# Performance work log

Measured on AMD Instinct MI355X. Metric: run time of the kernel, lower is better.

The kernel has to match this reference:

```python
import jax, jax.numpy as jnp
import numpy as np

B, T, DM = 2, 2048, 1024
H, HKV, DH = 16, 4, 64          # n_heads, n_kv_heads, head_dim
LAT, DFF = 64, 4096             # MLA latent dim, SwiGLU hidden (4*d_model)
SCALE = DH ** -0.5
ROPE_BASE = 10000.0


def _rope(x):
    # x: [B, T, h, DH]; split-half rotary
    half = DH // 2
    pos = jnp.arange(T, dtype=jnp.float32)
    inv_freq = 1.0 / (ROPE_BASE ** (jnp.arange(half, dtype=jnp.float32) / half))
    ang = pos[:, None] * inv_freq                      # [T, half]
    cos = jnp.cos(ang)[None, :, None, :]
    sin = jnp.sin(ang)[None, :, None, :]
    x1, x2 = x[..., :half], x[..., half:]
    return jnp.concatenate([x1 * cos - x2 * sin, x2 * cos + x1 * sin], axis=-1)


def setup_inputs() -> dict:
    key = jax.random.key(0)
    ks = jax.random.split(key, 9)
    init = lambda k, shape, fan: jax.random.normal(k, shape, jnp.float32) * (fan ** -0.5)
    return {
        "x": jax.random.normal(ks[0], (B, T, DM), jnp.float32),
        "Wq": init(ks[1], (DM, DM), DM),
        "Wkv_down": init(ks[2], (DM, LAT), DM),
        "Wk_up": init(ks[3], (LAT, HKV * DH), LAT),
        "Wv_up": init(ks[4], (LAT, HKV * DH), LAT),
        "Wgate": init(ks[5], (DH, DH), DH),
        "bgate": jnp.zeros((DH,), jnp.float32),
        "Wo1": init(ks[6], (DM, DFF), DM),
        "Wo2": init(ks[7], (DFF, DM), DFF),
    }


def reference(x, Wq, Wkv_down, Wk_up, Wv_up, Wgate, bgate, Wo1, Wo2):
    # GQA projections; MLA: shared low-rank latent -> K/V up-projections
    q = (x @ Wq).reshape(B, T, H, DH)
    lat = x @ Wkv_down                                  # [B, T, LAT]
    k = (lat @ Wk_up).reshape(B, T, HKV, DH)
    v = (lat @ Wv_up).reshape(B, T, HKV, DH)

    q = _rope(q)
    k = _rope(k)

    # repeat KV heads (GQA): kv head g serves q heads [g*rep, (g+1)*rep)
    rep = H // HKV
    k = jnp.repeat(k, rep, axis=2)                      # [B, T, H, DH]
    v = jnp.repeat(v, rep, axis=2)

    scores = jnp.einsum("bthd,bshd->bhts", q, k) * SCALE
    causal = jnp.tril(jnp.ones((T, T), dtype=bool))
    scores = jnp.where(causal[None, None], scores, -jnp.inf)
    attn = jax.nn.softmax(scores, axis=-1)
    out = jnp.einsum("bhts,bshd->bthd", attn, v)        # [B, T, H, DH]

    # Gated attention (G1, per_head): sigmoid gate after attention
    gate = jax.nn.sigmoid(out @ Wgate + bgate)
    out = (out * gate).reshape(B, T, DM)

    # SwiGLU-style out_proj: Linear -> SiLU -> Linear
    h = jax.nn.silu(out @ Wo1)
    return h @ Wo2
```

## Files before the change

kernel.cpp:

```cpp
#include <hip/hip_runtime.h>
#include <math.h>

#define NB 2
#define NT 2048
#define NDM 1024
#define NH 16
#define NHKV 4
#define NDH 64
#define NLAT 64
#define NDFF 4096

typedef __attribute__((ext_vector_type(4))) float fx4;
typedef __attribute__((ext_vector_type(8))) short bf8;
typedef __attribute__((ext_vector_type(4))) unsigned short us4;
typedef __attribute__((ext_vector_type(8))) unsigned short us8;

__device__ __forceinline__ unsigned short f2bf(float f) {
  union { float f; unsigned int u; } v; v.f = f;
  unsigned int u = v.u;
  u += 0x7fffu + ((u >> 16) & 1u);
  return (unsigned short)(u >> 16);
}

__global__ void conv_bf_k(const float* __restrict__ in,
                          unsigned short* __restrict__ out, int n8) {
  int idx = blockIdx.x * 256 + threadIdx.x;
  if (idx >= n8) return;
  fx4 a = *(const fx4*)(in + (size_t)idx * 8);
  fx4 b = *(const fx4*)(in + (size_t)idx * 8 + 4);
  us8 o = { f2bf(a[0]), f2bf(a[1]), f2bf(a[2]), f2bf(a[3]),
            f2bf(b[0]), f2bf(b[1]), f2bf(b[2]), f2bf(b[3]) };
  *(us8*)(out + (size_t)idx * 8) = o;
}

__global__ __launch_bounds__(256) void convT_bf_k(const float* __restrict__ W,
                                                  unsigned short* __restrict__ Wt,
                                                  int K, int N) {
  __shared__ float tile[64 * 65];
  const int t = threadIdx.x;
  const int k0 = blockIdx.x * 64, n0 = blockIdx.y * 64;
#pragma unroll
  for (int i = 0; i < 4; ++i) {
    int id = t + 256 * i;
    int row = id >> 4, c = (id & 15) * 4;
    fx4 v = *(const fx4*)(W + (size_t)(k0 + row) * N + n0 + c);
    tile[row * 65 + c + 0] = v[0];
    tile[row * 65 + c + 1] = v[1];
    tile[row * 65 + c + 2] = v[2];
    tile[row * 65 + c + 3] = v[3];
  }
  __syncthreads();
  const int nr = t >> 2, kc = (t & 3) * 16;
  us8 o0, o1;
#pragma unroll
  for (int e = 0; e < 8; ++e) o0[e] = f2bf(tile[(kc + e) * 65 + nr]);
#pragma unroll
  for (int e = 0; e < 8; ++e) o1[e] = f2bf(tile[(kc + 8 + e) * 65 + nr]);
  *(us8*)(Wt + (size_t)(n0 + nr) * K + k0 + kc) = o0;
  *(us8*)(Wt + (size_t)(n0 + nr) * K + k0 + kc + 8) = o1;
}

template<int EPI>
__global__ __launch_bounds__(256) void gemm_bf_k(const unsigned short* __restrict__ A,
                                                 const unsigned short* __restrict__ Bt,
                                                 void* __restrict__ Cp,
                                                 int M, int N, int K) {
  __shared__ unsigned short As[128 * 72];
  __shared__ unsigned short Bs[128 * 72];
  const int t = threadIdx.x;
  const int m0 = blockIdx.x * 128, n0 = blockIdx.y * 128;
  const int lane = t & 63, w = t >> 6;
  const int n = lane & 15, g = lane >> 4;
  const int wr = w >> 1, wc = w & 1;
  const int sw = (n & 7) << 3;
  fx4 acc[4][4];
#pragma unroll
  for (int mt = 0; mt < 4; ++mt)
#pragma unroll
    for (int nt = 0; nt < 4; ++nt) acc[mt][nt] = fx4{0.f, 0.f, 0.f, 0.f};

  for (int k0 = 0; k0 < K; k0 += 64) {
    __syncthreads();
#pragma unroll
    for (int i = 0; i < 4; ++i) {
      int id = t + 256 * i;
      int row = id >> 3, c = id & 7;
      int posa = 32 * (c >> 2) + 16 * (c & 1) + 4 * ((c >> 1) & 1);
      int swr = (row & 7) << 3;
      us8 av = *(const us8*)(A + (size_t)(m0 + row) * K + k0 + 8 * c);
      *(us4*)(As + row * 72 + (posa ^ swr))       = us4{av[0], av[1], av[2], av[3]};
      *(us4*)(As + row * 72 + ((posa + 8) ^ swr)) = us4{av[4], av[5], av[6], av[7]};
      us8 bv = *(const us8*)(Bt + (size_t)(n0 + row) * K + k0 + 8 * c);
      *(us4*)(Bs + row * 72 + (posa ^ swr))       = us4{bv[0], bv[1], bv[2], bv[3]};
      *(us4*)(Bs + row * 72 + ((posa + 8) ^ swr)) = us4{bv[4], bv[5], bv[6], bv[7]};
    }
    __syncthreads();
#pragma unroll
    for (int ks = 0; ks < 2; ++ks) {
      bf8 af[4], bfr[4];
#pragma unroll
      for (int mt = 0; mt < 4; ++mt) {
        int row = wr * 64 + mt * 16 + n;
        af[mt] = *(const bf8*)(As + row * 72 + ((32 * ks + 8 * g) ^ sw));
      }
#pragma unroll
      for (int nt = 0; nt < 4; ++nt) {
        int row = wc * 64 + nt * 16 + n;
        bfr[nt] = *(const bf8*)(Bs + row * 72 + ((32 * ks + 8 * g) ^ sw));
      }
#pragma unroll
      for (int mt = 0; mt < 4; ++mt)
#pragma unroll
        for (int nt = 0; nt < 4; ++nt)
          acc[mt][nt] = __builtin_amdgcn_mfma_f32_16x16x32_bf16(af[mt], bfr[nt], acc[mt][nt], 0, 0, 0);
    }
  }
#pragma unroll
  for (int mt = 0; mt < 4; ++mt)
#pragma unroll
    for (int nt = 0; nt < 4; ++nt)
#pragma unroll
      for (int r = 0; r < 4; ++r) {
        int row = m0 + wr * 64 + mt * 16 + 4 * g + r;
        int col = n0 + wc * 64 + nt * 16 + n;
        float v = acc[mt][nt][r];
        if (EPI == 1) {
          float s = v / (1.f + __expf(-v));
          ((unsigned short*)Cp)[(size_t)row * N + col] = f2bf(s);
        } else {
          ((float*)Cp)[(size_t)row * N + col] = v;
        }
      }
}

template<int ABF16, int EPI>
__global__ __launch_bounds__(256) void gemm_k(const void* __restrict__ Ap,
                                              const float* __restrict__ Bp,
                                              void* __restrict__ Cp,
                                              int M, int N, int K) {
  constexpr int LDK = 68;
  __shared__ unsigned short As[64 * LDK];
  __shared__ unsigned short Bs[64 * LDK];
  const int t = threadIdx.x;
  const int m0 = blockIdx.x * 64, n0 = blockIdx.y * 64;
  const int lane = t & 63, w = t >> 6;
  const int m16 = lane & 15, g = lane >> 4;
  const int arow = w * 16 + m16;
  fx4 acc[4] = {{0.f,0.f,0.f,0.f},{0.f,0.f,0.f,0.f},{0.f,0.f,0.f,0.f},{0.f,0.f,0.f,0.f}};

  for (int k0 = 0; k0 < K; k0 += 64) {
    __syncthreads();
#pragma unroll
    for (int i = 0; i < 4; ++i) {
      int id = t * 4 + i;
      int row = id >> 4, cg = (id & 15) * 4;
      if (ABF16) {
        const unsigned short* A = (const unsigned short*)Ap;
        *(us4*)(As + row * LDK + cg) =
            *(const us4*)(A + (size_t)(m0 + row) * K + k0 + cg);
      } else {
        const float* A = (const float*)Ap;
        fx4 a = *(const fx4*)(A + (size_t)(m0 + row) * K + k0 + cg);
        us4 ab = { f2bf(a[0]), f2bf(a[1]), f2bf(a[2]), f2bf(a[3]) };
        *(us4*)(As + row * LDK + cg) = ab;
      }
      fx4 bv = *(const fx4*)(Bp + (size_t)(k0 + row) * N + n0 + cg);
      Bs[(cg + 0) * LDK + row] = f2bf(bv[0]);
      Bs[(cg + 1) * LDK + row] = f2bf(bv[1]);
      Bs[(cg + 2) * LDK + row] = f2bf(bv[2]);
      Bs[(cg + 3) * LDK + row] = f2bf(bv[3]);
    }
    __syncthreads();
#pragma unroll
    for (int ks = 0; ks < 2; ++ks) {
      const int kb = ks * 32;
      us4 a0 = *(const us4*)(As + arow * LDK + kb + 4 * g);
      us4 a1 = *(const us4*)(As + arow * LDK + kb + 16 + 4 * g);
      bf8 af;
      af[0] = (short)a0[0]; af[1] = (short)a0[1]; af[2] = (short)a0[2]; af[3] = (short)a0[3];
      af[4] = (short)a1[0]; af[5] = (short)a1[1]; af[6] = (short)a1[2]; af[7] = (short)a1[3];
#pragma unroll
      for (int nt = 0; nt < 4; ++nt) {
        const int brow = nt * 16 + m16;
        us4 b0 = *(const us4*)(Bs + brow * LDK + kb + 4 * g);
        us4 b1 = *(const us4*)(Bs + brow * LDK + kb + 16 + 4 * g);
        bf8 bf_;
        bf_[0] = (short)b0[0]; bf_[1] = (short)b0[1]; bf_[2] = (short)b0[2]; bf_[3] = (short)b0[3];
        bf_[4] = (short)b1[0]; bf_[5] = (short)b1[1]; bf_[6] = (short)b1[2]; bf_[7] = (short)b1[3];
        acc[nt] = __builtin_amdgcn_mfma_f32_16x16x32_bf16(af, bf_, acc[nt], 0, 0, 0);
      }
    }
  }
#pragma unroll
  for (int nt = 0; nt < 4; ++nt) {
#pragma unroll
    for (int r = 0; r < 4; ++r) {
      int row = m0 + w * 16 + 4 * g + r;
      int col = n0 + nt * 16 + m16;
      float vv = acc[nt][r];
      if (EPI == 1) {
        float s = vv / (1.f + __expf(-vv));
        ((unsigned short*)Cp)[(size_t)row * N + col] = f2bf(s);
      } else {
        ((float*)Cp)[(size_t)row * N + col] = vv;
      }
    }
  }
}

__global__ void rope_k(float* __restrict__ x, int nheads, int total) {
  int idx = blockIdx.x * 256 + threadIdx.x;
  if (idx >= total) return;
  int i = idx & 31;
  int rest = idx >> 5;
  int tpos = (rest / nheads) % NT;
  float* p = x + (size_t)rest * NDH;
  float ang = (float)tpos * powf(10000.0f, -(float)i * (1.0f / 32.0f));
  float sn, cs;
  sincosf(ang, &sn, &cs);
  float x1 = p[i], x2 = p[i + 32];
  p[i]      = x1 * cs - x2 * sn;
  p[i + 32] = x2 * cs + x1 * sn;
}

__global__ __launch_bounds__(256) void attn_mfma_k(const float* __restrict__ qb,
                                                   const float* __restrict__ kb,
                                                   const float* __restrict__ vb,
                                                   const float* __restrict__ Wg,
                                                   const float* __restrict__ bg,
                                                   unsigned short* __restrict__ outp) {
  __shared__ __align__(16) char smem[45056];
  unsigned short* Qs = (unsigned short*)smem;
  unsigned short* Ks = Qs + 64 * 72;
  unsigned short* Vt = Ks + 64 * 72;
  float* wgs  = (float*)(smem + 27648);
  float* outs = (float*)smem;

  const int t = threadIdx.x;
  const int q0 = blockIdx.x * 64;
  const int bh = blockIdx.y;
  const int b = bh >> 4, h = bh & 15, kvh = h >> 2;
  const int lane = t & 63, wq = t >> 6;
  const int n = lane & 15, g = lane >> 4;
  const int sw = (n & 7) << 3;

#pragma unroll
  for (int i = 0; i < 16; ++i) {
    int id = t + 256 * i;
    wgs[(id >> 6) * 68 + (id & 63)] = Wg[id];
  }
#pragma unroll
  for (int i = 0; i < 4; ++i) {
    int id = t + 256 * i;
    int row = id >> 4, c = id & 15;
    fx4 a = *(const fx4*)(qb + (((size_t)b * NT + q0 + row) * NH + h) * NDH + 4 * c);
    int pos = 32 * (c >> 3) + 8 * (c & 3) + 4 * ((c >> 2) & 1);
    us4 ab = { f2bf(a[0]), f2bf(a[1]), f2bf(a[2]), f2bf(a[3]) };
    *(us4*)(Qs + row * 72 + (pos ^ ((row & 7) << 3))) = ab;
  }
  __syncthreads();

  const int qrow_l = wq * 16 + n;
  bf8 bq0 = *(const bf8*)(Qs + qrow_l * 72 + ((8 * g) ^ sw));
  bf8 bq1 = *(const bf8*)(Qs + qrow_l * 72 + ((32 | (8 * g)) ^ sw));

  float mrun = -INFINITY, lsum = 0.f;
  fx4 oacc[4] = {{0.f,0.f,0.f,0.f},{0.f,0.f,0.f,0.f},{0.f,0.f,0.f,0.f},{0.f,0.f,0.f,0.f}};

  for (int s0 = 0; s0 <= q0; s0 += 64) {
    __syncthreads();
#pragma unroll
    for (int i = 0; i < 4; ++i) {
      int id = t + 256 * i;
      int row = id >> 4, c = id & 15;
      const size_t base = (((size_t)b * NT + s0 + row) * NHKV + kvh) * NDH + 4 * c;
      fx4 kvv = *(const fx4*)(kb + base);
      int pos = 32 * (c >> 3) + 8 * (c & 3) + 4 * ((c >> 2) & 1);
      us4 ab = { f2bf(kvv[0]), f2bf(kvv[1]), f2bf(kvv[2]), f2bf(kvv[3]) };
      *(us4*)(Ks + row * 72 + (pos ^ ((row & 7) << 3))) = ab;
      fx4 vv = *(const fx4*)(vb + base);
      int sposr = 32 * (row >> 5) + 8 * ((row & 15) >> 2) + 4 * ((row >> 4) & 1) + (row & 3);
#pragma unroll
      for (int e = 0; e < 4; ++e) {
        int d = 4 * c + e;
        Vt[d * 72 + (sposr ^ ((d & 7) << 3))] = f2bf(vv[e]);
      }
    }
    __syncthreads();

    float sc[16];
#pragma unroll
    for (int nt = 0; nt < 4; ++nt) {
      const int krow = 16 * nt + n;
      bf8 ka0 = *(const bf8*)(Ks + krow * 72 + ((8 * g) ^ sw));
      bf8 ka1 = *(const bf8*)(Ks + krow * 72 + ((32 | (8 * g)) ^ sw));
      fx4 s4 = {0.f, 0.f, 0.f, 0.f};
      s4 = __builtin_amdgcn_mfma_f32_16x16x32_bf16(ka0, bq0, s4, 0, 0, 0);
      s4 = __builtin_amdgcn_mfma_f32_16x16x32_bf16(ka1, bq1, s4, 0, 0, 0);
#pragma unroll
      for (int r = 0; r < 4; ++r) sc[nt * 4 + r] = s4[r] * 0.125f;
    }
    if (s0 == q0) {
#pragma unroll
      for (int nt = 0; nt < 4; ++nt)
#pragma unroll
        for (int r = 0; r < 4; ++r)
          if (16 * nt + 4 * g + r > wq * 16 + n) sc[nt * 4 + r] = -INFINITY;
    }

    float tm = sc[0];
#pragma unroll
    for (int i = 1; i < 16; ++i) tm = fmaxf(tm, sc[i]);
    tm = fmaxf(tm, __shfl_xor(tm, 16));
    tm = fmaxf(tm, __shfl_xor(tm, 32));
    float mnew = fmaxf(mrun, tm);
    float corr = __expf(mrun - mnew);
    float p[16];
    float ls = 0.f;
#pragma unroll
    for (int i = 0; i < 16; ++i) { p[i] = __expf(sc[i] - mnew); ls += p[i]; }
    ls += __shfl_xor(ls, 16);
    ls += __shfl_xor(ls, 32);
    lsum = lsum * corr + ls;
    mrun = mnew;
#pragma unroll
    for (int dt = 0; dt < 4; ++dt) oacc[dt] *= corr;

    bf8 pb0, pb1;
#pragma unroll
    for (int j = 0; j < 8; ++j) {
      pb0[j] = (short)f2bf(p[j]);
      pb1[j] = (short)f2bf(p[8 + j]);
    }

#pragma unroll
    for (int dt = 0; dt < 4; ++dt) {
      const int vrow = 16 * dt + n;
      bf8 va0 = *(const bf8*)(Vt + vrow * 72 + ((8 * g) ^ sw));
      bf8 va1 = *(const bf8*)(Vt + vrow * 72 + ((32 | (8 * g)) ^ sw));
      oacc[dt] = __builtin_amdgcn_mfma_f32_16x16x32_bf16(va0, pb0, oacc[dt], 0, 0, 0);
      oacc[dt] = __builtin_amdgcn_mfma_f32_16x16x32_bf16(va1, pb1, oacc[dt], 0, 0, 0);
    }
  }

  __syncthreads();
  const float inv = 1.0f / lsum;
#pragma unroll
  for (int dt = 0; dt < 4; ++dt)
#pragma unroll
    for (int r = 0; r < 4; ++r)
      outs[(16 * wq + n) * 68 + 16 * dt + 4 * g + r] = oacc[dt][r] * inv;
  __syncthreads();

  const int r = t >> 2, qd = t & 3;
  fx4 gs[4];
#pragma unroll
  for (int j = 0; j < 4; ++j) gs[j] = *(const fx4*)(bg + qd * 16 + j * 4);
  for (int d = 0; d < 64; ++d) {
    float od = outs[r * 68 + d];
    const float* wr = wgs + d * 68 + qd * 16;
#pragma unroll
    for (int j = 0; j < 4; ++j) gs[j] += *(const fx4*)(wr + j * 4) * od;
  }
  unsigned short* op = outp + ((size_t)b * NT + q0 + r) * NDM + h * NDH + qd * 16;
#pragma unroll
  for (int j = 0; j < 4; ++j) {
    fx4 o = *(const fx4*)(outs + r * 68 + qd * 16 + j * 4);
    us4 rb;
#pragma unroll
    for (int e = 0; e < 4; ++e) {
      float gv = 1.f / (1.f + __expf(-gs[j][e]));
      rb[e] = f2bf(o[e] * gv);
    }
    *(us4*)(op + j * 4) = rb;
  }
}

extern "C" void kernel_launch(void* const* d_in, const int* in_sizes, int n_in,
                              void* d_out, int out_size, void* d_ws, size_t ws_size,
                              hipStream_t stream) {
  const float* x    = (const float*)d_in[0];
  const float* Wq   = (const float*)d_in[1];
  const float* Wkvd = (const float*)d_in[2];
  const float* Wku  = (const float*)d_in[3];
  const float* Wvu  = (const float*)d_in[4];
  const float* Wg   = (const float*)d_in[5];
  const float* bg   = (const float*)d_in[6];
  const float* Wo1  = (const float*)d_in[7];
  const float* Wo2  = (const float*)d_in[8];
  float* out = (float*)d_out;
  char* ws = (char*)d_ws;

  float*          q     = (float*)(ws);
  float*          lat   = (float*)(ws + 16777216);
  float*          kk    = (float*)(ws + 17825792);
  float*          vv    = (float*)(ws + 22020096);
  unsigned short* xb    = (unsigned short*)(ws + 26214400);
  unsigned short* hbuf  = (unsigned short*)(ws);
  unsigned short* WqT   = (unsigned short*)(ws + 34602880);
  unsigned short* Wo1T  = (unsigned short*)(ws + 36700160);
  unsigned short* Wo2T  = (unsigned short*)(ws + 45088768);
  unsigned short* aob   = (unsigned short*)(ws + 53477376);

  const int MT = NB * NT;
  dim3 blk(256);

  conv_bf_k<<<dim3(MT * NDM / 8 / 256), blk, 0, stream>>>(x, xb, MT * NDM / 8);
  convT_bf_k<<<dim3(NDM / 64, NDM / 64),  blk, 0, stream>>>(Wq,  WqT,  NDM, NDM);
  convT_bf_k<<<dim3(NDM / 64, NDFF / 64), blk, 0, stream>>>(Wo1, Wo1T, NDM, NDFF);
  convT_bf_k<<<dim3(NDFF / 64, NDM / 64), blk, 0, stream>>>(Wo2, Wo2T, NDFF, NDM);

  gemm_bf_k<0><<<dim3(MT/128, NDM/128), blk, 0, stream>>>(xb, WqT, (void*)q, MT, NDM, NDM);
  gemm_k<0,0><<<dim3(MT/64, NLAT/64), blk, 0, stream>>>((const void*)x,   Wkvd, (void*)lat, MT, NLAT,      NDM);
  gemm_k<0,0><<<dim3(MT/64, (NHKV*NDH)/64), blk, 0, stream>>>((const void*)lat, Wku, (void*)kk, MT, NHKV*NDH, NLAT);
  gemm_k<0,0><<<dim3(MT/64, (NHKV*NDH)/64), blk, 0, stream>>>((const void*)lat, Wvu, (void*)vv, MT, NHKV*NDH, NLAT);

  int qpairs = NB * NT * NH * 32;
  int kpairs = NB * NT * NHKV * 32;
  rope_k<<<dim3((qpairs + 255) / 256), blk, 0, stream>>>(q,  NH,   qpairs);
  rope_k<<<dim3((kpairs + 255) / 256), blk, 0, stream>>>(kk, NHKV, kpairs);

  attn_mfma_k<<<dim3(NT/64, NB*NH), blk, 0, stream>>>(q, kk, vv, Wg, bg, aob);

  gemm_bf_k<1><<<dim3(MT/128, NDFF/128), blk, 0, stream>>>(aob,  Wo1T, (void*)hbuf, MT, NDFF, NDM);
  gemm_bf_k<0><<<dim3(MT/128, NDM/128),  blk, 0, stream>>>(hbuf, Wo2T, (void*)out,  MT, NDM,  NDFF);
}
```

Measured before the change: 534.0 us.

## Use direct global-to-LDS loads in GEMM and restructure attention LDS layouts

The GEMM now stages A and B tiles with global_load_lds, which copies global memory straight into shared memory with an XOR-swizzled 64-wide row layout, and reads MFMA fragments through a new helper. The attention kernel stops swizzling Q/K, transposes V with lane shuffles into vectorized LDS stores instead of scalar scattered writes, and keeps the gate weights in bf16 to cut shared memory use. The aim is lower register and VALU staging cost and more occupancy. In exchange, bf16 gate weights lose precision, and the unswizzled layouts may cause LDS bank conflicts.

```diff
diff --git a/kernel.cpp b/kernel.cpp
--- a/kernel.cpp
+++ b/kernel.cpp
@@ -20,6 +20,9 @@
   unsigned int u = v.u;
   u += 0x7fffu + ((u >> 16) & 1u);
   return (unsigned short)(u >> 16);
+}
+__device__ __forceinline__ float bf2f(unsigned short h) {
+  union { unsigned u; float f; } v; v.u = ((unsigned)h) << 16; return v.f;
 }
 
 __global__ void conv_bf_k(const float* __restrict__ in,
@@ -60,19 +63,33 @@
   *(us8*)(Wt + (size_t)(n0 + nr) * K + k0 + kc + 8) = o1;
 }
 
+__device__ __forceinline__ bf8 fragG(const unsigned short* base, int row, int gr) {
+  const unsigned short* rb = base + row * 64;
+  const int r7 = row & 7;
+  us4 lo = *(const us4*)(rb + 8 * ((gr >> 1) ^ r7) + 4 * (gr & 1));
+  us4 hi = *(const us4*)(rb + 8 * (((gr + 4) >> 1) ^ r7) + 4 * (gr & 1));
+  bf8 f;
+  f[0] = (short)lo[0]; f[1] = (short)lo[1]; f[2] = (short)lo[2]; f[3] = (short)lo[3];
+  f[4] = (short)hi[0]; f[5] = (short)hi[1]; f[6] = (short)hi[2]; f[7] = (short)hi[3];
+  return f;
+}
+
 template<int EPI>
 __global__ __launch_bounds__(256) void gemm_bf_k(const unsigned short* __restrict__ A,
                                                  const unsigned short* __restrict__ Bt,
                                                  void* __restrict__ Cp,
                                                  int M, int N, int K) {
-  __shared__ unsigned short As[128 * 72];
-  __shared__ unsigned short Bs[128 * 72];
+  __shared__ __align__(16) unsigned short As[128 * 64];
+  __shared__ __align__(16) unsigned short Bs[128 * 64];
   const int t = threadIdx.x;
   const int m0 = blockIdx.x * 128, n0 = blockIdx.y * 128;
   const int lane = t & 63, w = t >> 6;
   const int n = lane & 15, g = lane >> 4;
   const int wr = w >> 1, wc = w & 1;
-  const int sw = (n & 7) << 3;
+  const int lrow = lane >> 3;
+  const int lslot = (lane & 7) ^ lrow;
+  const unsigned short* srcA = A  + (size_t)(m0 + 32 * w + lrow) * K + 8 * lslot;
+  const unsigned short* srcB = Bt + (size_t)(n0 + 32 * w + lrow) * K + 8 * lslot;
   fx4 acc[4][4];
 #pragma unroll
   for (int mt = 0; mt < 4; ++mt)
@@ -82,32 +99,26 @@
   for (int k0 = 0; k0 < K; k0 += 64) {
     __syncthreads();
 #pragma unroll
-    for (int i = 0; i < 4; ++i) {
-      int id = t + 256 * i;
-      int row = id >> 3, c = id & 7;
-      int posa = 32 * (c >> 2) + 16 * (c & 1) + 4 * ((c >> 1) & 1);
-      int swr = (row & 7) << 3;
-      us8 av = *(const us8*)(A + (size_t)(m0 + row) * K + k0 + 8 * c);
-      *(us4*)(As + row * 72 + (posa ^ swr))       = us4{av[0], av[1], av[2], av[3]};
-      *(us4*)(As + row * 72 + ((posa + 8) ^ swr)) = us4{av[4], av[5], av[6], av[7]};
-      us8 bv = *(const us8*)(Bt + (size_t)(n0 + row) * K + k0 + 8 * c);
-      *(us4*)(Bs + row * 72 + (posa ^ swr))       = us4{bv[0], bv[1], bv[2], bv[3]};
-      *(us4*)(Bs + row * 72 + ((posa + 8) ^ swr)) = us4{bv[4], bv[5], bv[6], bv[7]};
+    for (int u = 0; u < 4; ++u) {
+      __builtin_amdgcn_global_load_lds(
+          (const __attribute__((address_space(1))) unsigned int*)(srcA + (size_t)(8 * u) * K + k0),
+          (__attribute__((address_space(3))) unsigned int*)(As + (32 * w + 8 * u) * 64),
+          16, 0, 0);
+      __builtin_amdgcn_global_load_lds(
+          (const __attribute__((address_space(1))) unsigned int*)(srcB + (size_t)(8 * u) * K + k0),
+          (__attribute__((address_space(3))) unsigned int*)(Bs + (32 * w + 8 * u) * 64),
+          16, 0, 0);
     }
     __syncthreads();
 #pragma unroll
     for (int ks = 0; ks < 2; ++ks) {
       bf8 af[4], bfr[4];
 #pragma unroll
-      for (int mt = 0; mt < 4; ++mt) {
-        int row = wr * 64 + mt * 16 + n;
-        af[mt] = *(const bf8*)(As + row * 72 + ((32 * ks + 8 * g) ^ sw));
-      }
-#pragma unroll
-      for (int nt = 0; nt < 4; ++nt) {
-        int row = wc * 64 + nt * 16 + n;
-        bfr[nt] = *(const bf8*)(Bs + row * 72 + ((32 * ks + 8 * g) ^ sw));
-      }
+      for (int mt = 0; mt < 4; ++mt)
+        af[mt] = fragG(As, wr * 64 + mt * 16 + n, 8 * ks + g);
+#pragma unroll
+      for (int nt = 0; nt < 4; ++nt)
+        bfr[nt] = fragG(Bs, wc * 64 + nt * 16 + n, 8 * ks + g);
 #pragma unroll
       for (int mt = 0; mt < 4; ++mt)
 #pragma unroll
@@ -223,17 +234,36 @@
   p[i + 32] = x2 * cs + x1 * sn;
 }
 
+__device__ __forceinline__ bf8 frag64(const unsigned short* base, int row, int gr) {
+  const unsigned short* rb = base + row * 72;
+  us4 lo = *(const us4*)(rb + 4 * gr);
+  us4 hi = *(const us4*)(rb + 4 * gr + 16);
+  bf8 f;
+  f[0] = (short)lo[0]; f[1] = (short)lo[1]; f[2] = (short)lo[2]; f[3] = (short)lo[3];
+  f[4] = (short)hi[0]; f[5] = (short)hi[1]; f[6] = (short)hi[2]; f[7] = (short)hi[3];
+  return f;
+}
+__device__ __forceinline__ bf8 frag64v(const unsigned short* base, int row, int gr) {
+  const unsigned short* rb = base + row * 72 + 8 * ((row >> 3) & 1);
+  us4 lo = *(const us4*)(rb + 4 * gr);
+  us4 hi = *(const us4*)(rb + 4 * gr + 16);
+  bf8 f;
+  f[0] = (short)lo[0]; f[1] = (short)lo[1]; f[2] = (short)lo[2]; f[3] = (short)lo[3];
+  f[4] = (short)hi[0]; f[5] = (short)hi[1]; f[6] = (short)hi[2]; f[7] = (short)hi[3];
+  return f;
+}
+
 __global__ __launch_bounds__(256) void attn_mfma_k(const float* __restrict__ qb,
                                                    const float* __restrict__ kb,
                                                    const float* __restrict__ vb,
                                                    const float* __restrict__ Wg,
                                                    const float* __restrict__ bg,
                                                    unsigned short* __restrict__ outp) {
-  __shared__ __align__(16) char smem[45056];
-  unsigned short* Qs = (unsigned short*)smem;
-  unsigned short* Ks = Qs + 64 * 72;
-  unsigned short* Vt = Ks + 64 * 72;
-  float* wgs  = (float*)(smem + 27648);
+  __shared__ __align__(16) char smem[36352];
+  unsigned short* Qs  = (unsigned short*)smem;
+  unsigned short* Ks  = Qs + 64 * 72;
+  unsigned short* Vt  = Ks + 64 * 72;
+  unsigned short* wgs = Vt + 64 * 72;
   float* outs = (float*)smem;
 
   const int t = threadIdx.x;
@@ -242,27 +272,25 @@
   const int b = bh >> 4, h = bh & 15, kvh = h >> 2;
   const int lane = t & 63, wq = t >> 6;
   const int n = lane & 15, g = lane >> 4;
-  const int sw = (n & 7) << 3;
-
-#pragma unroll
-  for (int i = 0; i < 16; ++i) {
-    int id = t + 256 * i;
-    wgs[(id >> 6) * 68 + (id & 63)] = Wg[id];
-  }
+  const int srow = 4 * wq + g;
+  const int c = n;
+
 #pragma unroll
   for (int i = 0; i < 4; ++i) {
     int id = t + 256 * i;
-    int row = id >> 4, c = id & 15;
-    fx4 a = *(const fx4*)(qb + (((size_t)b * NT + q0 + row) * NH + h) * NDH + 4 * c);
-    int pos = 32 * (c >> 3) + 8 * (c & 3) + 4 * ((c >> 2) & 1);
+    int row = id >> 4, cc = id & 15;
+    fx4 wv = *(const fx4*)(Wg + (size_t)id * 4);
+    us4 wb = { f2bf(wv[0]), f2bf(wv[1]), f2bf(wv[2]), f2bf(wv[3]) };
+    *(us4*)(wgs + row * 68 + 4 * cc) = wb;
+    fx4 a = *(const fx4*)(qb + (((size_t)b * NT + q0 + row) * NH + h) * NDH + 4 * cc);
     us4 ab = { f2bf(a[0]), f2bf(a[1]), f2bf(a[2]), f2bf(a[3]) };
-    *(us4*)(Qs + row * 72 + (pos ^ ((row & 7) << 3))) = ab;
+    *(us4*)(Qs + row * 72 + 4 * cc) = ab;
   }
   __syncthreads();
 
   const int qrow_l = wq * 16 + n;
-  bf8 bq0 = *(const bf8*)(Qs + qrow_l * 72 + ((8 * g) ^ sw));
-  bf8 bq1 = *(const bf8*)(Qs + qrow_l * 72 + ((32 | (8 * g)) ^ sw));
+  bf8 bq0 = frag64(Qs, qrow_l, g);
+  bf8 bq1 = frag64(Qs, qrow_l, g + 8);
 
   float mrun = -INFINITY, lsum = 0.f;
   fx4 oacc[4] = {{0.f,0.f,0.f,0.f},{0.f,0.f,0.f,0.f},{0.f,0.f,0.f,0.f},{0.f,0.f,0.f,0.f}};
@@ -271,20 +299,24 @@
     __syncthreads();
 #pragma unroll
     for (int i = 0; i < 4; ++i) {
-      int id = t + 256 * i;
-      int row = id >> 4, c = id & 15;
+      const int row = srow + 16 * i;
       const size_t base = (((size_t)b * NT + s0 + row) * NHKV + kvh) * NDH + 4 * c;
-      fx4 kvv = *(const fx4*)(kb + base);
-      int pos = 32 * (c >> 3) + 8 * (c & 3) + 4 * ((c >> 2) & 1);
-      us4 ab = { f2bf(kvv[0]), f2bf(kvv[1]), f2bf(kvv[2]), f2bf(kvv[3]) };
-      *(us4*)(Ks + row * 72 + (pos ^ ((row & 7) << 3))) = ab;
-      fx4 vv = *(const fx4*)(vb + base);
-      int sposr = 32 * (row >> 5) + 8 * ((row & 15) >> 2) + 4 * ((row >> 4) & 1) + (row & 3);
-#pragma unroll
-      for (int e = 0; e < 4; ++e) {
-        int d = 4 * c + e;
-        Vt[d * 72 + (sposr ^ ((d & 7) << 3))] = f2bf(vv[e]);
-      }
+      fx4 kv4 = *(const fx4*)(kb + base);
+      us4 ab = { f2bf(kv4[0]), f2bf(kv4[1]), f2bf(kv4[2]), f2bf(kv4[3]) };
+      *(us4*)(Ks + row * 72 + 4 * c) = ab;
+
+      fx4 vv4 = *(const fx4*)(vb + base);
+      float u0 = vv4[0], u1 = vv4[1], u2 = vv4[2], u3 = vv4[3];
+      float t0 = __shfl_xor((g & 2) ? u0 : u2, 32);
+      float t1 = __shfl_xor((g & 2) ? u1 : u3, 32);
+      if (g & 2) { u0 = t0; u1 = t1; } else { u2 = t0; u3 = t1; }
+      float s0v = __shfl_xor((g & 1) ? u0 : u1, 16);
+      float s1v = __shfl_xor((g & 1) ? u2 : u3, 16);
+      if (g & 1) { u0 = s0v; u2 = s1v; } else { u1 = s0v; u3 = s1v; }
+      const int dd = 4 * c + g;
+      const int r0 = 4 * wq + 16 * i;
+      us4 tv = { f2bf(u0), f2bf(u1), f2bf(u2), f2bf(u3) };
+      *(us4*)(Vt + dd * 72 + 8 * ((dd >> 3) & 1) + r0) = tv;
     }
     __syncthreads();
 
@@ -292,8 +324,8 @@
 #pragma unroll
     for (int nt = 0; nt < 4; ++nt) {
       const int krow = 16 * nt + n;
-      bf8 ka0 = *(const bf8*)(Ks + krow * 72 + ((8 * g) ^ sw));
-      bf8 ka1 = *(const bf8*)(Ks + krow * 72 + ((32 | (8 * g)) ^ sw));
+      bf8 ka0 = frag64(Ks, krow, g);
+      bf8 ka1 = frag64(Ks, krow, g + 8);
       fx4 s4 = {0.f, 0.f, 0.f, 0.f};
       s4 = __builtin_amdgcn_mfma_f32_16x16x32_bf16(ka0, bq0, s4, 0, 0, 0);
       s4 = __builtin_amdgcn_mfma_f32_16x16x32_bf16(ka1, bq1, s4, 0, 0, 0);
@@ -336,8 +368,8 @@
 #pragma unroll
     for (int dt = 0; dt < 4; ++dt) {
       const int vrow = 16 * dt + n;
-      bf8 va0 = *(const bf8*)(Vt + vrow * 72 + ((8 * g) ^ sw));
-      bf8 va1 = *(const bf8*)(Vt + vrow * 72 + ((32 | (8 * g)) ^ sw));
+      bf8 va0 = frag64v(Vt, vrow, g);
+      bf8 va1 = frag64v(Vt, vrow, g + 8);
       oacc[dt] = __builtin_amdgcn_mfma_f32_16x16x32_bf16(va0, pb0, oacc[dt], 0, 0, 0);
       oacc[dt] = __builtin_amdgcn_mfma_f32_16x16x32_bf16(va1, pb1, oacc[dt], 0, 0, 0);
     }
@@ -358,9 +390,15 @@
   for (int j = 0; j < 4; ++j) gs[j] = *(const fx4*)(bg + qd * 16 + j * 4);
   for (int d = 0; d < 64; ++d) {
     float od = outs[r * 68 + d];
-    const float* wr = wgs + d * 68 + qd * 16;
-#pragma unroll
-    for (int j = 0; j < 4; ++j) gs[j] += *(const fx4*)(wr + j * 4) * od;
+    const unsigned short* wr = wgs + d * 68 + qd * 16;
+#pragma unroll
+    for (int j = 0; j < 4; ++j) {
+      us4 wv = *(const us4*)(wr + j * 4);
+      gs[j][0] += bf2f(wv[0]) * od;
+      gs[j][1] += bf2f(wv[1]) * od;
+      gs[j][2] += bf2f(wv[2]) * od;
+      gs[j][3] += bf2f(wv[3]) * od;
+    }
   }
   unsigned short* op = outp + ((size_t)b * NT + q0 + r) * NDM + h * NDH + qd * 16;
 #pragma unroll
```

Measured after the change: 459.0 us. 14.0% less time.
